# Kernel tuning notes

Hardware: AMD Instinct MI355X
Metric: run time of the kernel (lower is better)

## Reference

```python
import jax, jax.numpy as jnp
import numpy as np

N_NODES = 50000
N_EDGES = 800000
NEG_SLOPE = 0.2  # PyG GATConv default


def _gat_layer(x, src, dst, n, W, a_src, a_dst, b, concat):
    """One GATConv layer (PyG semantics, eval mode so attention dropout is off).

    x: [N, F_in], src/dst: [E'] (self loops included), W: [F_in, H*C],
    a_src/a_dst: [H, C], b: [H*C] if concat else [C].
    """
    H, C = a_src.shape
    h = (x @ W).reshape(n, H, C)                      # [N, H, C]
    al_s = jnp.sum(h * a_src, axis=-1)                # [N, H]
    al_d = jnp.sum(h * a_dst, axis=-1)                # [N, H]
    e = jax.nn.leaky_relu(al_s[src] + al_d[dst], NEG_SLOPE)  # [E', H]
    # numerically stable softmax over incoming edges of each dst node
    m = jax.lax.stop_gradient(jax.ops.segment_max(e, dst, num_segments=n))
    m = jnp.where(jnp.isfinite(m), m, 0.0)
    ex = jnp.exp(e - m[dst])                          # [E', H]
    denom = jax.ops.segment_sum(ex, dst, num_segments=n)     # [N, H]
    alpha = ex / denom[dst]                           # safe: self loops => denom > 0
    out = jax.ops.segment_sum(alpha[:, :, None] * h[src], dst, num_segments=n)  # [N,H,C]
    out = out.reshape(n, H * C) if concat else out.mean(axis=1)
    return out + b


def setup_inputs() -> dict:
    key = jax.random.key(0)
    ks = jax.random.split(key, 8)
    in_dim, hid, heads, out_dim = 256, 32, 8, 16
    x = jax.random.normal(ks[0], (N_NODES, in_dim), dtype=jnp.float32)
    edge_index = jax.random.randint(ks[1], (2, N_EDGES), 0, N_NODES, dtype=jnp.int64)
    s1 = 1.0 / np.sqrt(in_dim)
    s2 = 1.0 / np.sqrt(heads * hid)
    return {
        "x": x,
        "edge_index": edge_index,
        "W1": jax.random.normal(ks[2], (in_dim, heads * hid), dtype=jnp.float32) * s1,
        "a_src1": jax.random.normal(ks[3], (heads, hid), dtype=jnp.float32) * s2,
        "a_dst1": jax.random.normal(ks[4], (heads, hid), dtype=jnp.float32) * s2,
        "b1": jnp.zeros((heads * hid,), dtype=jnp.float32),
        "W2": jax.random.normal(ks[5], (heads * hid, out_dim), dtype=jnp.float32) * s2,
        "a_src2": jax.random.normal(ks[6], (1, out_dim), dtype=jnp.float32) * 0.25,
        "a_dst2": jax.random.normal(ks[7], (1, out_dim), dtype=jnp.float32) * 0.25,
        "b2": jnp.zeros((out_dim,), dtype=jnp.float32),
    }


def reference(x, edge_index, W1, a_src1, a_dst1, b1, W2, a_src2, a_dst2, b2):
    n = x.shape[0]
    loops = jnp.arange(n, dtype=edge_index.dtype)
    src = jnp.concatenate([edge_index[0], loops])  # add_self_loops (PyG default)
    dst = jnp.concatenate([edge_index[1], loops])
    h = jax.nn.relu(_gat_layer(x, src, dst, n, W1, a_src1, a_dst1, b1, concat=True))
    # F.dropout(p=0.5, training=False) -> identity in eval mode
    h = _gat_layer(h, src, dst, n, W2, a_src2, a_dst2, b2, concat=False)
    return jax.nn.log_softmax(h, axis=1)
```

## Files before the change

kernel.cpp:

```cpp
#include <hip/hip_runtime.h>
#include <hip/hip_bf16.h>


#define LRELU(x) ((x) > 0.f ? (x) : 0.2f * (x))

typedef __attribute__((ext_vector_type(8))) short short8;
typedef __attribute__((ext_vector_type(8))) unsigned short ushort8;
typedef __attribute__((ext_vector_type(4))) float f32x4;

__device__ inline unsigned short f2b(float f) {
    __hip_bfloat16 h = __float2bfloat16(f);
    return *reinterpret_cast<unsigned short*>(&h);
}
__device__ inline float b2f(unsigned short u) {
    __hip_bfloat16 h;
    *reinterpret_cast<unsigned short*>(&h) = u;
    return __bfloat162float(h);
}


__global__ void k_hist(const int* __restrict__ dst, int* deg, int E) {
    int i = blockIdx.x * blockDim.x + threadIdx.x;
    if (i < E) atomicAdd(&deg[dst[i]], 1);
}

__global__ __launch_bounds__(256) void k_scanA(const int* __restrict__ deg,
                                               int* __restrict__ tmp,
                                               int* __restrict__ blocksum, int n) {
    __shared__ int sc[256];
    int b = blockIdx.x, t = threadIdx.x;
    int i = b * 256 + t;
    int v = (i < n) ? deg[i] + 1 : 0;
    sc[t] = v;
    __syncthreads();
    for (int off = 1; off < 256; off <<= 1) {
        int x = 0;
        if (t >= off) x = sc[t - off];
        __syncthreads();
        sc[t] += x;
        __syncthreads();
    }
    if (i < n) tmp[i] = sc[t] - v;
    if (t == 255) blocksum[b] = sc[255];
}

__global__ __launch_bounds__(256) void k_scanB(const int* __restrict__ blocksum,
                                               int* __restrict__ blockpre, int nb) {
    __shared__ int sc[256];
    int t = threadIdx.x;
    int v = (t < nb) ? blocksum[t] : 0;
    sc[t] = v;
    __syncthreads();
    for (int off = 1; off < 256; off <<= 1) {
        int x = 0;
        if (t >= off) x = sc[t - off];
        __syncthreads();
        sc[t] += x;
        __syncthreads();
    }
    if (t < nb) blockpre[t] = sc[t] - v;
}

__global__ __launch_bounds__(256) void k_scanC(const int* __restrict__ tmp,
                                               const int* __restrict__ blockpre,
                                               int* __restrict__ offs,
                                               int* __restrict__ cursor, int n, int P) {
    int b = blockIdx.x, t = threadIdx.x;
    int i = b * 256 + t;
    if (i < n) {
        int o = tmp[i] + blockpre[b];
        offs[i] = o;
        cursor[i] = o;
    }
    if (i == 0) offs[n] = P;
}

__global__ void k_scatter(const int* __restrict__ src, const int* __restrict__ dst,
                          int* cursor, int* __restrict__ csr, int E, int n) {
    int i = blockIdx.x * blockDim.x + threadIdx.x;
    int s, d;
    if (i < E) {
        s = src[i];
        d = dst[i];
    } else if (i < E + n) {
        s = i - E;
        d = s;
    } else {
        return;
    }
    int p = atomicAdd(&cursor[d], 1);
    csr[p] = s;
}


__global__ __launch_bounds__(256) void k_prepw(const float* __restrict__ W,
                                               unsigned short* __restrict__ Wt) {
    int k = blockIdx.x;
    int nn = threadIdx.x;
    Wt[nn * 256 + k] = f2b(W[k * 256 + nn]);
}

__global__ __launch_bounds__(256) void k_prepw2(const float* __restrict__ W,
                                                unsigned short* __restrict__ Wt) {
    int nn = blockIdx.x;
    int k = threadIdx.x;
    Wt[nn * 256 + k] = f2b(W[k * 16 + nn]);
}


__global__ __launch_bounds__(256) void k_gemm1(const float* __restrict__ A,
                                               const unsigned short* __restrict__ Wt,
                                               unsigned short* __restrict__ h1b, int M) {
    __shared__ unsigned short As[128][40];
    __shared__ unsigned short Bs[128][40];
    int t = threadIdx.x;
    int r0 = blockIdx.x * 128, c0 = blockIdx.y * 128;
    int srow = t >> 1, shalf = t & 1;
    int lane = t & 63, w = t >> 6;
    int lane15 = lane & 15, quad = lane >> 4;
    int rbw = (w & 1) * 64, cbw = (w >> 1) * 64;

    f32x4 acc[4][4];
#pragma unroll
    for (int i = 0; i < 4; i++)
#pragma unroll
        for (int j = 0; j < 4; j++) acc[i][j] = (f32x4)0.f;

    for (int k0 = 0; k0 < 256; k0 += 32) {
        {
            int row = r0 + srow;
            ushort8 p0, p1;
            if (row < M) {
                const float4* sp = (const float4*)&A[(size_t)row * 256 + k0 + shalf * 16];
                float4 f0 = sp[0], f1 = sp[1], f2 = sp[2], f3 = sp[3];
                p0[0] = f2b(f0.x); p0[1] = f2b(f0.y); p0[2] = f2b(f0.z); p0[3] = f2b(f0.w);
                p0[4] = f2b(f1.x); p0[5] = f2b(f1.y); p0[6] = f2b(f1.z); p0[7] = f2b(f1.w);
                p1[0] = f2b(f2.x); p1[1] = f2b(f2.y); p1[2] = f2b(f2.z); p1[3] = f2b(f2.w);
                p1[4] = f2b(f3.x); p1[5] = f2b(f3.y); p1[6] = f2b(f3.z); p1[7] = f2b(f3.w);
            } else {
                p0 = (ushort8)0; p1 = (ushort8)0;
            }
            *(ushort8*)&As[srow][shalf * 16] = p0;
            *(ushort8*)&As[srow][shalf * 16 + 8] = p1;
            const ushort8* bp = (const ushort8*)&Wt[(size_t)(c0 + srow) * 256 + k0 + shalf * 16];
            *(ushort8*)&Bs[srow][shalf * 16] = bp[0];
            *(ushort8*)&Bs[srow][shalf * 16 + 8] = bp[1];
        }
        __syncthreads();
        short8 af[4], bf[4];
#pragma unroll
        for (int i = 0; i < 4; i++)
            af[i] = *(const short8*)&As[rbw + i * 16 + lane15][quad * 8];
#pragma unroll
        for (int j = 0; j < 4; j++)
            bf[j] = *(const short8*)&Bs[cbw + j * 16 + lane15][quad * 8];
#pragma unroll
        for (int i = 0; i < 4; i++)
#pragma unroll
            for (int j = 0; j < 4; j++)
                acc[i][j] = __builtin_amdgcn_mfma_f32_16x16x32_bf16(af[i], bf[j], acc[i][j], 0, 0, 0);
        __syncthreads();
    }
#pragma unroll
    for (int i = 0; i < 4; i++) {
        int rowb = r0 + rbw + i * 16 + quad * 4;
#pragma unroll
        for (int j = 0; j < 4; j++) {
            int col = c0 + cbw + j * 16 + lane15;
#pragma unroll
            for (int r = 0; r < 4; r++) {
                int row = rowb + r;
                if (row < M) h1b[(size_t)row * 256 + col] = f2b(acc[i][j][r]);
            }
        }
    }
}


__global__ __launch_bounds__(256) void k_al1(const unsigned short* __restrict__ h1b,
                                             const float* __restrict__ asrc,
                                             const float* __restrict__ adst,
                                             float* __restrict__ als,
                                             float* __restrict__ ald, int n) {
    int v = blockIdx.x * 4 + (threadIdx.x >> 6);
    if (v >= n) return;
    int lane = threadIdx.x & 63;
    const uint2* hp = (const uint2*)(h1b + (size_t)v * 256);
    uint2 pk = hp[lane];
    float f0 = __uint_as_float(pk.x << 16);
    float f1 = __uint_as_float(pk.x & 0xffff0000u);
    float f2 = __uint_as_float(pk.y << 16);
    float f3 = __uint_as_float(pk.y & 0xffff0000u);
    float4 a_s = ((const float4*)asrc)[lane];
    float4 a_d = ((const float4*)adst)[lane];
    float ps = f0 * a_s.x + f1 * a_s.y + f2 * a_s.z + f3 * a_s.w;
    float pd = f0 * a_d.x + f1 * a_d.y + f2 * a_d.z + f3 * a_d.w;
#pragma unroll
    for (int off = 1; off < 8; off <<= 1) {
        ps += __shfl_xor(ps, off, 64);
        pd += __shfl_xor(pd, off, 64);
    }
    if ((lane & 7) == 0) {
        int h = lane >> 3;
        als[v * 8 + h] = ps;
        ald[v * 8 + h] = pd;
    }
}


__global__ __launch_bounds__(128) void k_agg1(const int* __restrict__ csr,
                                              const int* __restrict__ offs,
                                              const float* __restrict__ als,
                                              const float* __restrict__ aldg,
                                              const unsigned short* __restrict__ h1b,
                                              const float* __restrict__ b1,
                                              unsigned short* __restrict__ x2b) {
    int v = blockIdx.x;
    int t = threadIdx.x;
    int start = offs[v];
    int deg = offs[v + 1] - start;
    __shared__ float aldv[8];
    __shared__ int su[32];
    __shared__ float ws[8 * 33];
    if (t < 8) aldv[t] = aldg[v * 8 + t];
    __syncthreads();
    int h = t >> 4;
    const unsigned int* __restrict__ hbase = (const unsigned int*)h1b;
    float a0 = 0.f, a1 = 0.f, wsum = 0.f;
    for (int base = 0; base < deg; base += 32) {
        int cnt = min(32, deg - base);
        int cnt4 = (cnt + 3) & ~3;
        if (base) __syncthreads();
        if (t < cnt4) {
            if (t < cnt) {
                int u = csr[start + base + t];
                su[t] = u;
                const float4* ap = (const float4*)(als + (size_t)u * 8);
                float4 x0 = ap[0], x1 = ap[1];
                ws[0 * 33 + t] = __expf(LRELU(x0.x + aldv[0]));
                ws[1 * 33 + t] = __expf(LRELU(x0.y + aldv[1]));
                ws[2 * 33 + t] = __expf(LRELU(x0.z + aldv[2]));
                ws[3 * 33 + t] = __expf(LRELU(x0.w + aldv[3]));
                ws[4 * 33 + t] = __expf(LRELU(x1.x + aldv[4]));
                ws[5 * 33 + t] = __expf(LRELU(x1.y + aldv[5]));
                ws[6 * 33 + t] = __expf(LRELU(x1.z + aldv[6]));
                ws[7 * 33 + t] = __expf(LRELU(x1.w + aldv[7]));
            } else {
                su[t] = v;
#pragma unroll
                for (int k = 0; k < 8; k++) ws[k * 33 + t] = 0.f;
            }
        }
        __syncthreads();
        for (int e = 0; e < cnt4; e += 4) {
            int u0 = su[e + 0], u1 = su[e + 1], u2 = su[e + 2], u3 = su[e + 3];
            float w0 = ws[h * 33 + e + 0];
            float w1 = ws[h * 33 + e + 1];
            float w2 = ws[h * 33 + e + 2];
            float w3 = ws[h * 33 + e + 3];
            unsigned int pk0 = hbase[u0 * 128 + t];
            unsigned int pk1 = hbase[u1 * 128 + t];
            unsigned int pk2 = hbase[u2 * 128 + t];
            unsigned int pk3 = hbase[u3 * 128 + t];
            a0 += w0 * __uint_as_float(pk0 << 16);
            a1 += w0 * __uint_as_float(pk0 & 0xffff0000u);
            a0 += w1 * __uint_as_float(pk1 << 16);
            a1 += w1 * __uint_as_float(pk1 & 0xffff0000u);
            a0 += w2 * __uint_as_float(pk2 << 16);
            a1 += w2 * __uint_as_float(pk2 & 0xffff0000u);
            a0 += w3 * __uint_as_float(pk3 << 16);
            a1 += w3 * __uint_as_float(pk3 & 0xffff0000u);
            wsum += (w0 + w1) + (w2 + w3);
        }
    }
    const float2* b1v = (const float2*)b1;
    float2 bb = b1v[t];
    float inv = 1.0f / wsum;
    float o0 = a0 * inv + bb.x;
    float o1 = a1 * inv + bb.y;
    o0 = o0 > 0.f ? o0 : 0.f;
    o1 = o1 > 0.f ? o1 : 0.f;
    unsigned int opk = (unsigned int)f2b(o0) | ((unsigned int)f2b(o1) << 16);
    ((unsigned int*)(x2b + (size_t)v * 256))[t] = opk;
}


__global__ __launch_bounds__(256) void k_gemm2(const unsigned short* __restrict__ Xb,
                                               const unsigned short* __restrict__ W2t,
                                               const float* __restrict__ asrc,
                                               const float* __restrict__ adst,
                                               unsigned short* __restrict__ h2b,
                                               float* __restrict__ als,
                                               float* __restrict__ ald, int n) {
    int t = threadIdx.x;
    int lane = t & 63, w = t >> 6;
    int lane15 = lane & 15, quad = lane >> 4;
    int row0 = blockIdx.x * 64 + w * 16;
    f32x4 acc = (f32x4)0.f;
#pragma unroll
    for (int k0 = 0; k0 < 256; k0 += 32) {
        short8 a = *(const short8*)&Xb[(size_t)(row0 + lane15) * 256 + k0 + quad * 8];
        short8 b = *(const short8*)&W2t[lane15 * 256 + k0 + quad * 8];
        acc = __builtin_amdgcn_mfma_f32_16x16x32_bf16(a, b, acc, 0, 0, 0);
    }
    float asv = asrc[lane15], adv = adst[lane15];
#pragma unroll
    for (int r = 0; r < 4; r++) {
        int row = row0 + quad * 4 + r;
        float hv = acc[r];
        float ps = hv * asv, pd = hv * adv;
#pragma unroll
        for (int off = 1; off < 16; off <<= 1) {
            ps += __shfl_xor(ps, off, 16);
            pd += __shfl_xor(pd, off, 16);
        }
        if (row < n) {
            h2b[(size_t)row * 16 + lane15] = f2b(hv);
            if (lane15 == 0) {
                als[row] = ps;
                ald[row] = pd;
            }
        }
    }
}


__global__ __launch_bounds__(256) void k_agg2(const int* __restrict__ csr,
                                              const int* __restrict__ offs,
                                              const float* __restrict__ als,
                                              const float* __restrict__ aldg,
                                              const unsigned short* __restrict__ h2b,
                                              const float* __restrict__ b2,
                                              float* __restrict__ out, int n) {
    int v = blockIdx.x * 4 + (threadIdx.x >> 6);
    if (v >= n) return;
    int lane = threadIdx.x & 63;
    int start = offs[v];
    int deg = offs[v + 1] - start;
    float aldv = aldg[v];
    int c = lane & 15, q = lane >> 4;
    float acc = 0.f, wsum = 0.f;
    for (int e = q; e < deg; e += 4) {
        int u = csr[start + e];
        float x = als[u] + aldv;
        float wv = __expf(LRELU(x));
        acc += wv * b2f(h2b[(size_t)u * 16 + c]);
        wsum += wv;
    }
    acc += __shfl_xor(acc, 32, 64);
    acc += __shfl_xor(acc, 16, 64);
    wsum += __shfl_xor(wsum, 32, 64);
    wsum += __shfl_xor(wsum, 16, 64);
    float o = acc / wsum + b2[c];
    float mx = o;
#pragma unroll
    for (int off = 8; off; off >>= 1) mx = fmaxf(mx, __shfl_xor(mx, off, 16));
    float s = __expf(o - mx);
#pragma unroll
    for (int off = 8; off; off >>= 1) s += __shfl_xor(s, off, 16);
    float res = o - mx - __logf(s);
    if (q == 0) out[(size_t)v * 16 + c] = res;
}


extern "C" void kernel_launch(void* const* d_in, const int* in_sizes, int n_in,
                              void* d_out, int out_size, void* d_ws, size_t ws_size,
                              hipStream_t stream) {
    const float* x = (const float*)d_in[0];
    const int* ei = (const int*)d_in[1];
    const float* W1 = (const float*)d_in[2];
    const float* asrc1 = (const float*)d_in[3];
    const float* adst1 = (const float*)d_in[4];
    const float* b1 = (const float*)d_in[5];
    const float* W2 = (const float*)d_in[6];
    const float* asrc2 = (const float*)d_in[7];
    const float* adst2 = (const float*)d_in[8];
    const float* b2 = (const float*)d_in[9];
    float* out = (float*)d_out;

    int n = in_sizes[0] / 256;
    int E = in_sizes[1] / 2;
    int P = E + n;
    const int* src = ei;
    const int* dst = ei + E;
    int NB = (n + 255) / 256;

    char* p = (char*)d_ws;
    auto alloc = [&](size_t bytes) {
        void* r = (void*)p;
        p += (bytes + 255) & ~(size_t)255;
        return r;
    };
    unsigned short* h1b = (unsigned short*)alloc((size_t)n * 256 * 2);
    unsigned short* x2b = (unsigned short*)alloc((size_t)n * 256 * 2);
    unsigned short* W1t = (unsigned short*)alloc((size_t)256 * 256 * 2);
    unsigned short* W2t = (unsigned short*)alloc((size_t)16 * 256 * 2);
    float* als1 = (float*)alloc((size_t)n * 8 * 4);
    float* ald1 = (float*)alloc((size_t)n * 8 * 4);
    unsigned short* h2b = (unsigned short*)alloc((size_t)n * 16 * 2);
    float* als2 = (float*)alloc((size_t)n * 4);
    float* ald2 = (float*)alloc((size_t)n * 4);
    int* deg = (int*)alloc((size_t)n * 4);
    int* offs = (int*)alloc((size_t)(n + 1) * 4);
    int* cursor = (int*)alloc((size_t)n * 4);
    int* stmp = (int*)alloc((size_t)n * 4);
    int* blocksum = (int*)alloc((size_t)NB * 4);
    int* blockpre = (int*)alloc((size_t)NB * 4);
    int* csr = (int*)alloc((size_t)P * 4);

    hipMemsetAsync(deg, 0, (size_t)n * 4, stream);
    k_hist<<<(E + 255) / 256, 256, 0, stream>>>(dst, deg, E);
    k_scanA<<<NB, 256, 0, stream>>>(deg, stmp, blocksum, n);
    k_scanB<<<1, 256, 0, stream>>>(blocksum, blockpre, NB);
    k_scanC<<<NB, 256, 0, stream>>>(stmp, blockpre, offs, cursor, n, P);
    k_scatter<<<(P + 255) / 256, 256, 0, stream>>>(src, dst, cursor, csr, E, n);

    k_prepw<<<256, 256, 0, stream>>>(W1, W1t);
    k_prepw2<<<16, 256, 0, stream>>>(W2, W2t);
    k_gemm1<<<dim3((n + 127) / 128, 2), 256, 0, stream>>>(x, W1t, h1b, n);
    k_al1<<<(n + 3) / 4, 256, 0, stream>>>(h1b, asrc1, adst1, als1, ald1, n);
    k_agg1<<<n, 128, 0, stream>>>(csr, offs, als1, ald1, h1b, b1, x2b);

    k_gemm2<<<(n + 63) / 64, 256, 0, stream>>>(x2b, W2t, asrc2, adst2, h2b, als2, ald2, n);
    k_agg2<<<(n + 3) / 4, 256, 0, stream>>>(csr, offs, als2, ald2, h2b, b2, out, n);
}
```

Baseline: 333.4 us.

## Fuse attention logits into GEMM1 and merge small prep and scan kernels

GEMM1 now computes all 256 output columns per block (128x256 tile) and reduces the per-head attention dot products in its epilogue with shuffles, removing the separate k_al1 pass that re-read h1. The degree histogram and both weight transposes are merged into a single k_prep launch, and the single-block scanB is folded into scanC, where each block redundantly scans the block sums. This cuts launch count and one full read of h1, but doubles accumulator registers in GEMM1 (acc[4][8]) and halves the grid, which may lower occupancy.

```diff
diff --git a/kernel.cpp b/kernel.cpp
--- a/kernel.cpp
+++ b/kernel.cpp
@@ -19,10 +19,25 @@
 }
 
 
-__global__ void k_hist(const int* __restrict__ dst, int* deg, int E) {
-    int i = blockIdx.x * blockDim.x + threadIdx.x;
-    if (i < E) atomicAdd(&deg[dst[i]], 1);
-}
+__global__ __launch_bounds__(256) void k_prep(const int* __restrict__ dst, int* deg, int E,
+                                              const float* __restrict__ W1,
+                                              unsigned short* __restrict__ W1t,
+                                              const float* __restrict__ W2,
+                                              unsigned short* __restrict__ W2t,
+                                              int HB) {
+    int b = blockIdx.x, t = threadIdx.x;
+    if (b < HB) {
+        int i = b * 256 + t;
+        if (i < E) atomicAdd(&deg[dst[i]], 1);
+    } else if (b < HB + 256) {
+        int k = b - HB;
+        W1t[t * 256 + k] = f2b(W1[k * 256 + t]);
+    } else {
+        int nn = b - HB - 256;
+        W2t[nn * 256 + t] = f2b(W2[t * 16 + nn]);
+    }
+}
+
 
 __global__ __launch_bounds__(256) void k_scanA(const int* __restrict__ deg,
                                                int* __restrict__ tmp,
@@ -44,10 +59,15 @@
     if (t == 255) blocksum[b] = sc[255];
 }
 
-__global__ __launch_bounds__(256) void k_scanB(const int* __restrict__ blocksum,
-                                               int* __restrict__ blockpre, int nb) {
+
+__global__ __launch_bounds__(256) void k_scanC(const int* __restrict__ tmp,
+                                               const int* __restrict__ blocksum,
+                                               int* __restrict__ offs,
+                                               int* __restrict__ cursor,
+                                               int n, int P, int nb) {
     __shared__ int sc[256];
-    int t = threadIdx.x;
+    __shared__ int base;
+    int b = blockIdx.x, t = threadIdx.x;
     int v = (t < nb) ? blocksum[t] : 0;
     sc[t] = v;
     __syncthreads();
@@ -58,21 +78,15 @@
         sc[t] += x;
         __syncthreads();
     }
-    if (t < nb) blockpre[t] = sc[t] - v;
-}
-
-__global__ __launch_bounds__(256) void k_scanC(const int* __restrict__ tmp,
-                                               const int* __restrict__ blockpre,
-                                               int* __restrict__ offs,
-                                               int* __restrict__ cursor, int n, int P) {
-    int b = blockIdx.x, t = threadIdx.x;
+    if (t == 0) base = (b == 0) ? 0 : sc[b - 1];
+    __syncthreads();
     int i = b * 256 + t;
     if (i < n) {
-        int o = tmp[i] + blockpre[b];
+        int o = tmp[i] + base;
         offs[i] = o;
         cursor[i] = o;
     }
-    if (i == 0) offs[n] = P;
+    if (b == 0 && t == 0) offs[n] = P;
 }
 
 __global__ void k_scatter(const int* __restrict__ src, const int* __restrict__ dst,
@@ -93,38 +107,27 @@
 }
 
 
-__global__ __launch_bounds__(256) void k_prepw(const float* __restrict__ W,
-                                               unsigned short* __restrict__ Wt) {
-    int k = blockIdx.x;
-    int nn = threadIdx.x;
-    Wt[nn * 256 + k] = f2b(W[k * 256 + nn]);
-}
-
-__global__ __launch_bounds__(256) void k_prepw2(const float* __restrict__ W,
-                                                unsigned short* __restrict__ Wt) {
-    int nn = blockIdx.x;
-    int k = threadIdx.x;
-    Wt[nn * 256 + k] = f2b(W[k * 16 + nn]);
-}
-
-
 __global__ __launch_bounds__(256) void k_gemm1(const float* __restrict__ A,
                                                const unsigned short* __restrict__ Wt,
-                                               unsigned short* __restrict__ h1b, int M) {
+                                               unsigned short* __restrict__ h1b,
+                                               const float* __restrict__ asrc,
+                                               const float* __restrict__ adst,
+                                               float* __restrict__ als,
+                                               float* __restrict__ ald, int M) {
     __shared__ unsigned short As[128][40];
-    __shared__ unsigned short Bs[128][40];
+    __shared__ unsigned short Bs[256][40];
     int t = threadIdx.x;
-    int r0 = blockIdx.x * 128, c0 = blockIdx.y * 128;
+    int r0 = blockIdx.x * 128;
     int srow = t >> 1, shalf = t & 1;
     int lane = t & 63, w = t >> 6;
     int lane15 = lane & 15, quad = lane >> 4;
-    int rbw = (w & 1) * 64, cbw = (w >> 1) * 64;
-
-    f32x4 acc[4][4];
+    int rbw = (w & 1) * 64, cbw = (w >> 1) * 128;
+
+    f32x4 acc[4][8];
 #pragma unroll
     for (int i = 0; i < 4; i++)
 #pragma unroll
-        for (int j = 0; j < 4; j++) acc[i][j] = (f32x4)0.f;
+        for (int j = 0; j < 8; j++) acc[i][j] = (f32x4)0.f;
 
     for (int k0 = 0; k0 < 256; k0 += 32) {
         {
@@ -142,68 +145,65 @@
             }
             *(ushort8*)&As[srow][shalf * 16] = p0;
             *(ushort8*)&As[srow][shalf * 16 + 8] = p1;
-            const ushort8* bp = (const ushort8*)&Wt[(size_t)(c0 + srow) * 256 + k0 + shalf * 16];
-            *(ushort8*)&Bs[srow][shalf * 16] = bp[0];
-            *(ushort8*)&Bs[srow][shalf * 16 + 8] = bp[1];
-        }
-        __syncthreads();
-        short8 af[4], bf[4];
+            const ushort8* bp = (const ushort8*)&Wt[(size_t)t * 256 + k0];
+            *(ushort8*)&Bs[t][0] = bp[0];
+            *(ushort8*)&Bs[t][8] = bp[1];
+            *(ushort8*)&Bs[t][16] = bp[2];
+            *(ushort8*)&Bs[t][24] = bp[3];
+        }
+        __syncthreads();
+        short8 af[4], bf[8];
 #pragma unroll
         for (int i = 0; i < 4; i++)
             af[i] = *(const short8*)&As[rbw + i * 16 + lane15][quad * 8];
 #pragma unroll
-        for (int j = 0; j < 4; j++)
+        for (int j = 0; j < 8; j++)
             bf[j] = *(const short8*)&Bs[cbw + j * 16 + lane15][quad * 8];
 #pragma unroll
         for (int i = 0; i < 4; i++)
 #pragma unroll
-            for (int j = 0; j < 4; j++)
+            for (int j = 0; j < 8; j++)
                 acc[i][j] = __builtin_amdgcn_mfma_f32_16x16x32_bf16(af[i], bf[j], acc[i][j], 0, 0, 0);
         __syncthreads();
     }
+
+    float asv[8], adv[8];
+#pragma unroll
+    for (int j = 0; j < 8; j++) {
+        asv[j] = asrc[cbw + j * 16 + lane15];
+        adv[j] = adst[cbw + j * 16 + lane15];
+    }
+    int hbase0 = cbw >> 5;
 #pragma unroll
     for (int i = 0; i < 4; i++) {
         int rowb = r0 + rbw + i * 16 + quad * 4;
 #pragma unroll
-        for (int j = 0; j < 4; j++) {
-            int col = c0 + cbw + j * 16 + lane15;
+        for (int j = 0; j < 8; j++) {
+            int col = cbw + j * 16 + lane15;
 #pragma unroll
             for (int r = 0; r < 4; r++) {
                 int row = rowb + r;
                 if (row < M) h1b[(size_t)row * 256 + col] = f2b(acc[i][j][r]);
             }
         }
-    }
-}
-
-
-__global__ __launch_bounds__(256) void k_al1(const unsigned short* __restrict__ h1b,
-                                             const float* __restrict__ asrc,
-                                             const float* __restrict__ adst,
-                                             float* __restrict__ als,
-                                             float* __restrict__ ald, int n) {
-    int v = blockIdx.x * 4 + (threadIdx.x >> 6);
-    if (v >= n) return;
-    int lane = threadIdx.x & 63;
-    const uint2* hp = (const uint2*)(h1b + (size_t)v * 256);
-    uint2 pk = hp[lane];
-    float f0 = __uint_as_float(pk.x << 16);
-    float f1 = __uint_as_float(pk.x & 0xffff0000u);
-    float f2 = __uint_as_float(pk.y << 16);
-    float f3 = __uint_as_float(pk.y & 0xffff0000u);
-    float4 a_s = ((const float4*)asrc)[lane];
-    float4 a_d = ((const float4*)adst)[lane];
-    float ps = f0 * a_s.x + f1 * a_s.y + f2 * a_s.z + f3 * a_s.w;
-    float pd = f0 * a_d.x + f1 * a_d.y + f2 * a_d.z + f3 * a_d.w;
-#pragma unroll
-    for (int off = 1; off < 8; off <<= 1) {
-        ps += __shfl_xor(ps, off, 64);
-        pd += __shfl_xor(pd, off, 64);
-    }
-    if ((lane & 7) == 0) {
-        int h = lane >> 3;
-        als[v * 8 + h] = ps;
-        ald[v * 8 + h] = pd;
+#pragma unroll
+        for (int m = 0; m < 4; m++) {
+#pragma unroll
+            for (int r = 0; r < 4; r++) {
+                float ps = acc[i][2 * m][r] * asv[2 * m] + acc[i][2 * m + 1][r] * asv[2 * m + 1];
+                float pd = acc[i][2 * m][r] * adv[2 * m] + acc[i][2 * m + 1][r] * adv[2 * m + 1];
+#pragma unroll
+                for (int off = 1; off < 16; off <<= 1) {
+                    ps += __shfl_xor(ps, off, 16);
+                    pd += __shfl_xor(pd, off, 16);
+                }
+                int row = rowb + r;
+                if (lane15 == 0 && row < M) {
+                    als[(size_t)row * 8 + hbase0 + m] = ps;
+                    ald[(size_t)row * 8 + hbase0 + m] = pd;
+                }
+            }
+        }
     }
 }
 
@@ -384,6 +384,7 @@
     const int* src = ei;
     const int* dst = ei + E;
     int NB = (n + 255) / 256;
+    int HB = (E + 255) / 256;
 
     char* p = (char*)d_ws;
     auto alloc = [&](size_t bytes) {
@@ -405,20 +406,15 @@
     int* cursor = (int*)alloc((size_t)n * 4);
     int* stmp = (int*)alloc((size_t)n * 4);
     int* blocksum = (int*)alloc((size_t)NB * 4);
-    int* blockpre = (int*)alloc((size_t)NB * 4);
     int* csr = (int*)alloc((size_t)P * 4);
 
     hipMemsetAsync(deg, 0, (size_t)n * 4, stream);
-    k_hist<<<(E + 255) / 256, 256, 0, stream>>>(dst, deg, E);
+    k_prep<<<HB + 256 + 16, 256, 0, stream>>>(dst, deg, E, W1, W1t, W2, W2t, HB);
     k_scanA<<<NB, 256, 0, stream>>>(deg, stmp, blocksum, n);
-    k_scanB<<<1, 256, 0, stream>>>(blocksum, blockpre, NB);
-    k_scanC<<<NB, 256, 0, stream>>>(stmp, blockpre, offs, cursor, n, P);
+    k_scanC<<<NB, 256, 0, stream>>>(stmp, blocksum, offs, cursor, n, P, NB);
     k_scatter<<<(P + 255) / 256, 256, 0, stream>>>(src, dst, cursor, csr, E, n);
 
-    k_prepw<<<256, 256, 0, stream>>>(W1, W1t);
-    k_prepw2<<<16, 256, 0, stream>>>(W2, W2t);
-    k_gemm1<<<dim3((n + 127) / 128, 2), 256, 0, stream>>>(x, W1t, h1b, n);
-    k_al1<<<(n + 3) / 4, 256, 0, stream>>>(h1b, asrc1, adst1, als1, ald1, n);
+    k_gemm1<<<(n + 127) / 128, 256, 0, stream>>>(x, W1t, h1b, asrc1, adst1, als1, ald1, n);
     k_agg1<<<n, 128, 0, stream>>>(csr, offs, als1, ald1, h1b, b1, x2b);
 
     k_gemm2<<<(n + 63) / 64, 256, 0, stream>>>(x2b, W2t, asrc2, adst2, h2b, als2, ald2, n);
```

Measured after the change: 354.4 us. 6.3% more time.
